# Optimization experiments

Hardware: AMD Instinct MI355X
Metric: run time of the kernel (lower is better)

Reference implementation:

```python
import jax, jax.numpy as jnp
import numpy as np

B, TE, TD, H = 4, 1024, 512, 128


def setup_inputs() -> dict:
    key = jax.random.key(0)
    k1, k2, k3, k4, k5 = jax.random.split(key, 5)
    return {
        "encoder_out": jax.random.normal(k1, (B, TE, H), dtype=jnp.float32),
        "decoder_out": jax.random.normal(k2, (B, TD, H), dtype=jnp.float32),
        "W_a": jax.random.normal(k3, (H, H), dtype=jnp.float32) * 0.05,
        "U_a": jax.random.normal(k4, (H, H), dtype=jnp.float32) * 0.05,
        "V_a": jax.random.normal(k5, (H, 1), dtype=jnp.float32) * 0.05,
    }


def reference(encoder_out, decoder_out, W_a, U_a, V_a):
    # Bahdanau additive attention, vectorized over all decoder steps at once.
    # (The original K.rnn loop has no true recurrence; steps are independent.)
    W_s = jnp.einsum('bth,hk->btk', encoder_out, W_a)   # [B, Te, H]
    U_h = jnp.einsum('bdh,hk->bdk', decoder_out, U_a)   # [B, Td, H]
    # energies: v^T tanh(W s_t + U h_d) -> [B, Td, Te]
    tanh_arg = jnp.tanh(W_s[:, None, :, :] + U_h[:, :, None, :])  # [B, Td, Te, H]
    e = jnp.einsum('bdth,ho->bdt', tanh_arg, V_a)
    e = jax.nn.softmax(e, axis=-1)                      # attention weights [B, Td, Te]
    # context vectors: weighted sum over encoder positions -> [B, Td, H]
    c = jnp.einsum('bdt,bth->bdh', e, encoder_out)
    return (c, e)
```

## Files before the change

kernel.cpp:

```cpp
#include <hip/hip_runtime.h>

#define BB    4
#define TE    1024
#define TD    512
#define HH    128
#define DTILE 4
#define TTILE 64
#define ESTR  (TE + 8)
#define LOG2E 1.4426950408889634f

typedef float f32x2 __attribute__((ext_vector_type(2)));

__device__ __forceinline__ f32x2 pk_fma(f32x2 a, f32x2 b, f32x2 c) {
    return __builtin_elementwise_fma(a, b, c);
}

__device__ __forceinline__ float tanh_eval(float x) {
    float e = __builtin_amdgcn_exp2f(2.0f * LOG2E * x);
    return 1.0f - 2.0f * __builtin_amdgcn_rcpf(e + 1.0f);
}

__global__ __launch_bounds__(512) void proj_gemm(
    const float* __restrict__ enc, const float* __restrict__ dec,
    const float* __restrict__ Wa,  const float* __restrict__ Ua,
    float* __restrict__ out)
{
    __shared__ float Xs[16 * HH];

    const int tid = threadIdx.x;
    const int r0  = blockIdx.x * 16;

    const float* X; const float* W; int rX0;
    if (r0 < BB * TE) { X = enc; W = Wa; rX0 = r0; }
    else              { X = dec; W = Ua; rX0 = r0 - BB * TE; }

    {
        const int r = tid >> 5, c = tid & 31;
        *(float4*)&Xs[r * HH + c * 4] =
            *(const float4*)&X[(size_t)(rX0 + r) * HH + c * 4];
    }
    __syncthreads();

    const int rr = tid >> 5;
    const int c4 = tid & 31;

    f32x2 aL0 = {0.f, 0.f}, aH0 = {0.f, 0.f};
    f32x2 aL1 = {0.f, 0.f}, aH1 = {0.f, 0.f};

    const float* Wc   = W + c4 * 4;
    const float* xrow = &Xs[rr * HH];

    #pragma unroll 4
    for (int k = 0; k < HH; k += 4) {
        float4 w0 = *(const float4*)&Wc[(k + 0) * HH];
        float4 w1 = *(const float4*)&Wc[(k + 1) * HH];
        float4 w2 = *(const float4*)&Wc[(k + 2) * HH];
        float4 w3 = *(const float4*)&Wc[(k + 3) * HH];
        float4 xv = *(const float4*)&xrow[k];

        aL0 = pk_fma((f32x2){xv.x, xv.x}, (f32x2){w0.x, w0.y}, aL0);
        aH0 = pk_fma((f32x2){xv.x, xv.x}, (f32x2){w0.z, w0.w}, aH0);
        aL1 = pk_fma((f32x2){xv.y, xv.y}, (f32x2){w1.x, w1.y}, aL1);
        aH1 = pk_fma((f32x2){xv.y, xv.y}, (f32x2){w1.z, w1.w}, aH1);
        aL0 = pk_fma((f32x2){xv.z, xv.z}, (f32x2){w2.x, w2.y}, aL0);
        aH0 = pk_fma((f32x2){xv.z, xv.z}, (f32x2){w2.z, w2.w}, aH0);
        aL1 = pk_fma((f32x2){xv.w, xv.w}, (f32x2){w3.x, w3.y}, aL1);
        aH1 = pk_fma((f32x2){xv.w, xv.w}, (f32x2){w3.z, w3.w}, aH1);
    }

    f32x2 aL = aL0 + aL1;
    f32x2 aH = aH0 + aH1;

    float4 o;
    o.x = tanh_eval(aL.x); o.y = tanh_eval(aL.y);
    o.z = tanh_eval(aH.x); o.w = tanh_eval(aH.y);
    *(float4*)&out[(size_t)(r0 + rr) * HH + c4 * 4] = o;
}

__global__ __launch_bounds__(512, 4) void attn_fused(
    const float* __restrict__ enc,
    const float* __restrict__ ta,
    const float* __restrict__ tb,
    const float* __restrict__ Va,
    float* __restrict__ c_out,
    float* __restrict__ e_out)
{
    __shared__ float e_s[DTILE * ESTR];
    __shared__ float c_red[8 * DTILE * HH];

    const int tid = threadIdx.x;
    const int l   = tid & 63;
    const int w   = tid >> 6;
    const int b   = blockIdx.x >> 7;
    const int d0  = (blockIdx.x & 127) * DTILE;

    {
        const int g  = l >> 3;
        const int hl = l & 7;
        const int dl = g & 3;
        const int rh = g >> 2;

        f32x2 Bl[4], Bh[4], Pl[4], Ph[4], Vl[4], Vh[4];
        #pragma unroll
        for (int j = 0; j < 4; ++j) {
            float4 vv = *(const float4*)&Va[(j * 8 + hl) * 4];
            float4 bb = *(const float4*)&tb[((size_t)b * TD + d0 + dl) * HH + (j * 8 + hl) * 4];
            Vl[j] = (f32x2){vv.x, vv.y};  Vh[j] = (f32x2){vv.z, vv.w};
            Bl[j] = (f32x2){bb.x, bb.y};  Bh[j] = (f32x2){bb.z, bb.w};
            Pl[j] = Vl[j] * Bl[j];        Ph[j] = Vh[j] * Bh[j];
        }

        const float* ta_b = ta + (size_t)b * TE * HH;

        auto rowOf = [&](int i) {
            return ((i >> 2) << 6) + w * 8 + ((i & 3) << 1) + rh;
        };

        float4 A0[4], A1[4];
        auto loadA = [&](int i, float4 (&A)[4]) {
            const float* base = ta_b + (size_t)rowOf(i) * HH;
            #pragma unroll
            for (int j = 0; j < 4; ++j)
                A[j] = *(const float4*)&base[(j * 8 + hl) * 4];
        };

        auto p1c = [&](int i, float4 (&A)[4]) {
            const f32x2 one2 = {1.0f, 1.0f};
            f32x2 n2[8], d2[8];
            #pragma unroll
            for (int j = 0; j < 4; ++j) {
                f32x2 Al = (f32x2){A[j].x, A[j].y};
                f32x2 Ah = (f32x2){A[j].z, A[j].w};
                n2[2 * j]     = pk_fma(Vl[j], Al, Pl[j]);
                n2[2 * j + 1] = pk_fma(Vh[j], Ah, Ph[j]);
                d2[2 * j]     = pk_fma(Al, Bl[j], one2);
                d2[2 * j + 1] = pk_fma(Ah, Bh[j], one2);
            }
            #pragma unroll
            for (int s = 4; s >= 1; s >>= 1) {
                #pragma unroll
                for (int k = 0; k < s; ++k) {
                    n2[k] = pk_fma(n2[2 * k], d2[2 * k + 1], n2[2 * k + 1] * d2[2 * k]);
                    d2[k] = d2[2 * k] * d2[2 * k + 1];
                }
            }
            float num = n2[0].x * d2[0].y + n2[0].y * d2[0].x;
            float den = d2[0].x * d2[0].y;
            float e = num * __builtin_amdgcn_rcpf(den);
            e += __shfl_xor(e, 1);
            e += __shfl_xor(e, 2);
            e += __shfl_xor(e, 4);
            if (hl == 0) e_s[dl * ESTR + rowOf(i)] = e;
        };

        loadA(0, A0);
        #pragma unroll 1
        for (int i = 0; i < 62; i += 2) {
            loadA(i + 1, A1);
            p1c(i, A0);
            loadA(i + 2, A0);
            p1c(i + 1, A1);
        }
        loadA(63, A1);
        p1c(62, A0);
        p1c(63, A1);
    }
    __syncthreads();

    {
        const int d2 = w & 3, hf = w >> 2;
        float ev[16];
        float m = -3.0e38f;
        #pragma unroll
        for (int i = 0; i < 16; ++i) {
            ev[i] = e_s[d2 * ESTR + i * 64 + l];
            m = fmaxf(m, ev[i]);
        }
        #pragma unroll
        for (int off = 32; off; off >>= 1) m = fmaxf(m, __shfl_xor(m, off));
        float s = 0.f;
        #pragma unroll
        for (int i = 0; i < 16; ++i) {
            ev[i] = __builtin_amdgcn_exp2f((ev[i] - m) * LOG2E);
            s += ev[i];
        }
        #pragma unroll
        for (int off = 32; off; off >>= 1) s += __shfl_xor(s, off);
        float inv = __builtin_amdgcn_rcpf(s);

        __syncthreads();
        float* eo = e_out + ((size_t)b * TD + d0 + d2) * TE;
        #pragma unroll
        for (int i = 0; i < 8; ++i) {
            int ii = hf * 8 + i;
            float p = ev[ii] * inv;
            e_s[d2 * ESTR + ii * 64 + l] = p;
            eo[ii * 64 + l] = p;
        }
        __syncthreads();
    }

    const int h4 = l & 31, tsub = l >> 5;
    f32x2 accL[DTILE], accH[DTILE];
    #pragma unroll
    for (int d = 0; d < DTILE; ++d) {
        accL[d] = (f32x2){0.f, 0.f};
        accH[d] = (f32x2){0.f, 0.f};
    }

    {
        const float* enc_w = enc + ((size_t)b * TE + w * 8) * HH;
        float4 X0[4], X1[4];

        auto loadX = [&](int tt, float4 (&X)[4]) {
            const float* base = enc_w + (size_t)tt * TTILE * HH;
            #pragma unroll
            for (int k = 0; k < 4; ++k)
                X[k] = *(const float4*)&base[(tsub * 4 + k) * HH + h4 * 4];
        };

        auto p3c = [&](int tt, float4 (&X)[4]) {
            float4 ep[DTILE];
            #pragma unroll
            for (int d = 0; d < DTILE; ++d)
                ep[d] = *(const float4*)&e_s[d * ESTR + tt * TTILE + w * 8 + tsub * 4];
            #pragma unroll
            for (int k = 0; k < 4; ++k) {
                f32x2 xL = (f32x2){X[k].x, X[k].y};
                f32x2 xH = (f32x2){X[k].z, X[k].w};
                #pragma unroll
                for (int d = 0; d < DTILE; ++d) {
                    float p = k == 0 ? ep[d].x : k == 1 ? ep[d].y
                            : k == 2 ? ep[d].z : ep[d].w;
                    f32x2 pv = (f32x2){p, p};
                    accL[d] = pk_fma(pv, xL, accL[d]);
                    accH[d] = pk_fma(pv, xH, accH[d]);
                }
            }
        };

        loadX(0, X0);
        #pragma unroll 1
        for (int tt = 0; tt < 14; tt += 2) {
            loadX(tt + 1, X1);
            p3c(tt, X0);
            loadX(tt + 2, X0);
            p3c(tt + 1, X1);
        }
        loadX(15, X1);
        p3c(14, X0);
        p3c(15, X1);
    }

    float4 acc4[DTILE];
    #pragma unroll
    for (int d = 0; d < DTILE; ++d)
        acc4[d] = make_float4(accL[d].x, accL[d].y, accH[d].x, accH[d].y);
    #pragma unroll
    for (int d = 0; d < DTILE; ++d) {
        acc4[d].x += __shfl_xor(acc4[d].x, 32);
        acc4[d].y += __shfl_xor(acc4[d].y, 32);
        acc4[d].z += __shfl_xor(acc4[d].z, 32);
        acc4[d].w += __shfl_xor(acc4[d].w, 32);
    }
    if (tsub == 0) {
        #pragma unroll
        for (int d = 0; d < DTILE; ++d)
            *(float4*)&c_red[(w * DTILE + d) * HH + h4 * 4] = acc4[d];
    }
    __syncthreads();

    if (w < DTILE && l < 32) {
        float4 o = make_float4(0.f, 0.f, 0.f, 0.f);
        #pragma unroll
        for (int ww = 0; ww < 8; ++ww) {
            float4 p = *(const float4*)&c_red[(ww * DTILE + w) * HH + l * 4];
            o.x += p.x; o.y += p.y; o.z += p.z; o.w += p.w;
        }
        *(float4*)&c_out[((size_t)b * TD + d0 + w) * HH + l * 4] = o;
    }
}

extern "C" void kernel_launch(void* const* d_in, const int* in_sizes, int n_in,
                              void* d_out, int out_size, void* d_ws, size_t ws_size,
                              hipStream_t stream) {
    (void)in_sizes; (void)n_in; (void)out_size; (void)ws_size;

    const float* enc = (const float*)d_in[0];
    const float* dec = (const float*)d_in[1];
    const float* Wa  = (const float*)d_in[2];
    const float* Ua  = (const float*)d_in[3];
    const float* Va  = (const float*)d_in[4];

    float* c_out = (float*)d_out;
    float* e_out = (float*)d_out + BB * TD * HH;

    float* proj = (float*)d_ws;
    float* ta_p = proj;
    float* tb_p = proj + BB * TE * HH;

    proj_gemm<<<384, 512, 0, stream>>>(enc, dec, Wa, Ua, proj);
    attn_fused<<<(BB * TD) / DTILE, 512, 0, stream>>>(enc, ta_p, tb_p, Va, c_out, e_out);
}
```

Measured before the change: 131.0 us.

## Double attention block threads and stagger projection K loop start

```diff
diff --git a/kernel.cpp b/kernel.cpp
--- a/kernel.cpp
+++ b/kernel.cpp
@@ -25,33 +25,24 @@
     const float* __restrict__ Wa,  const float* __restrict__ Ua,
     float* __restrict__ out)
 {
-    __shared__ float Xs[16 * HH];
-
     const int tid = threadIdx.x;
-    const int r0  = blockIdx.x * 16;
+    const int bid = blockIdx.x;
+    const int r0  = bid * 16;
 
     const float* X; const float* W; int rX0;
     if (r0 < BB * TE) { X = enc; W = Wa; rX0 = r0; }
     else              { X = dec; W = Ua; rX0 = r0 - BB * TE; }
 
-    {
-        const int r = tid >> 5, c = tid & 31;
-        *(float4*)&Xs[r * HH + c * 4] =
-            *(const float4*)&X[(size_t)(rX0 + r) * HH + c * 4];
-    }
-    __syncthreads();
-
     const int rr = tid >> 5;
     const int c4 = tid & 31;
 
+    const float* xrow = X + (size_t)(rX0 + rr) * HH;
+    const float* Wc   = W + c4 * 4;
+
     f32x2 aL0 = {0.f, 0.f}, aH0 = {0.f, 0.f};
     f32x2 aL1 = {0.f, 0.f}, aH1 = {0.f, 0.f};
 
-    const float* Wc   = W + c4 * 4;
-    const float* xrow = &Xs[rr * HH];
-
-    #pragma unroll 4
-    for (int k = 0; k < HH; k += 4) {
+    auto body = [&](int k) {
         float4 w0 = *(const float4*)&Wc[(k + 0) * HH];
         float4 w1 = *(const float4*)&Wc[(k + 1) * HH];
         float4 w2 = *(const float4*)&Wc[(k + 2) * HH];
@@ -66,7 +57,13 @@
         aH0 = pk_fma((f32x2){xv.z, xv.z}, (f32x2){w2.z, w2.w}, aH0);
         aL1 = pk_fma((f32x2){xv.w, xv.w}, (f32x2){w3.x, w3.y}, aL1);
         aH1 = pk_fma((f32x2){xv.w, xv.w}, (f32x2){w3.z, w3.w}, aH1);
-    }
+    };
+
+    const int k0 = (bid & 31) * 4;
+    #pragma unroll 4
+    for (int k = k0; k < HH; k += 4) body(k);
+    #pragma unroll 4
+    for (int k = 0; k < k0; k += 4) body(k);
 
     f32x2 aL = aL0 + aL1;
     f32x2 aH = aH0 + aH1;
@@ -77,7 +74,7 @@
     *(float4*)&out[(size_t)(r0 + rr) * HH + c4 * 4] = o;
 }
 
-__global__ __launch_bounds__(512, 4) void attn_fused(
+__global__ __launch_bounds__(1024, 8) void attn_fused(
     const float* __restrict__ enc,
     const float* __restrict__ ta,
     const float* __restrict__ tb,
@@ -86,7 +83,7 @@
     float* __restrict__ e_out)
 {
     __shared__ float e_s[DTILE * ESTR];
-    __shared__ float c_red[8 * DTILE * HH];
+    __shared__ float c_red[16 * DTILE * HH];
 
     const int tid = threadIdx.x;
     const int l   = tid & 63;
@@ -95,6 +92,8 @@
     const int d0  = (blockIdx.x & 127) * DTILE;
 
     {
+        const int w2 = w & 7;
+        const int ih = w >> 3;
         const int g  = l >> 3;
         const int hl = l & 7;
         const int dl = g & 3;
@@ -113,7 +112,7 @@
         const float* ta_b = ta + (size_t)b * TE * HH;
 
         auto rowOf = [&](int i) {
-            return ((i >> 2) << 6) + w * 8 + ((i & 3) << 1) + rh;
+            return ((i >> 2) << 6) + w2 * 8 + ((i & 3) << 1) + rh;
         };
 
         float4 A0[4], A1[4];
@@ -153,22 +152,23 @@
             if (hl == 0) e_s[dl * ESTR + rowOf(i)] = e;
         };
 
-        loadA(0, A0);
+        const int i0 = ih * 32;
+        loadA(i0, A0);
         #pragma unroll 1
-        for (int i = 0; i < 62; i += 2) {
+        for (int i = i0; i < i0 + 30; i += 2) {
             loadA(i + 1, A1);
             p1c(i, A0);
             loadA(i + 2, A0);
             p1c(i + 1, A1);
         }
-        loadA(63, A1);
-        p1c(62, A0);
-        p1c(63, A1);
+        loadA(i0 + 31, A1);
+        p1c(i0 + 30, A0);
+        p1c(i0 + 31, A1);
     }
     __syncthreads();
 
     {
-        const int d2 = w & 3, hf = w >> 2;
+        const int d2 = w & 3, q = w >> 2;
         float ev[16];
         float m = -3.0e38f;
         #pragma unroll
@@ -191,8 +191,8 @@
         __syncthreads();
         float* eo = e_out + ((size_t)b * TD + d0 + d2) * TE;
         #pragma unroll
-        for (int i = 0; i < 8; ++i) {
-            int ii = hf * 8 + i;
+        for (int i = 0; i < 4; ++i) {
+            int ii = q * 4 + i;
             float p = ev[ii] * inv;
             e_s[d2 * ESTR + ii * 64 + l] = p;
             eo[ii * 64 + l] = p;
@@ -209,29 +209,28 @@
     }
 
     {
-        const float* enc_w = enc + ((size_t)b * TE + w * 8) * HH;
-        float4 X0[4], X1[4];
-
-        auto loadX = [&](int tt, float4 (&X)[4]) {
+        const float* enc_w = enc + ((size_t)b * TE + w * 4) * HH;
+        float4 X0[2], X1[2];
+
+        auto loadX = [&](int tt, float4 (&Xr)[2]) {
             const float* base = enc_w + (size_t)tt * TTILE * HH;
             #pragma unroll
-            for (int k = 0; k < 4; ++k)
-                X[k] = *(const float4*)&base[(tsub * 4 + k) * HH + h4 * 4];
-        };
-
-        auto p3c = [&](int tt, float4 (&X)[4]) {
-            float4 ep[DTILE];
+            for (int k = 0; k < 2; ++k)
+                Xr[k] = *(const float4*)&base[(tsub * 2 + k) * HH + h4 * 4];
+        };
+
+        auto p3c = [&](int tt, float4 (&Xr)[2]) {
+            f32x2 ep[DTILE];
             #pragma unroll
             for (int d = 0; d < DTILE; ++d)
-                ep[d] = *(const float4*)&e_s[d * ESTR + tt * TTILE + w * 8 + tsub * 4];
-            #pragma unroll
-            for (int k = 0; k < 4; ++k) {
-                f32x2 xL = (f32x2){X[k].x, X[k].y};
-                f32x2 xH = (f32x2){X[k].z, X[k].w};
+                ep[d] = *(const f32x2*)&e_s[d * ESTR + tt * TTILE + w * 4 + tsub * 2];
+            #pragma unroll
+            for (int k = 0; k < 2; ++k) {
+                f32x2 xL = (f32x2){Xr[k].x, Xr[k].y};
+                f32x2 xH = (f32x2){Xr[k].z, Xr[k].w};
                 #pragma unroll
                 for (int d = 0; d < DTILE; ++d) {
-                    float p = k == 0 ? ep[d].x : k == 1 ? ep[d].y
-                            : k == 2 ? ep[d].z : ep[d].w;
+                    float p = (k == 0) ? ep[d].x : ep[d].y;
                     f32x2 pv = (f32x2){p, p};
                     accL[d] = pk_fma(pv, xL, accL[d]);
                     accH[d] = pk_fma(pv, xH, accH[d]);
@@ -273,7 +272,7 @@
     if (w < DTILE && l < 32) {
         float4 o = make_float4(0.f, 0.f, 0.f, 0.f);
         #pragma unroll
-        for (int ww = 0; ww < 8; ++ww) {
+        for (int ww = 0; ww < 16; ++ww) {
             float4 p = *(const float4*)&c_red[(ww * DTILE + w) * HH + l * 4];
             o.x += p.x; o.y += p.y; o.z += p.z; o.w += p.w;
         }
@@ -300,5 +299,5 @@
     float* tb_p = proj + BB * TE * HH;
 
     proj_gemm<<<384, 512, 0, stream>>>(enc, dec, Wa, Ua, proj);
-    attn_fused<<<(BB * TD) / DTILE, 512, 0, stream>>>(enc, ta_p, tb_p, Va, c_out, e_out);
-}
+    attn_fused<<<(BB * TD) / DTILE, 1024, 0, stream>>>(enc, ta_p, tb_p, Va, c_out, e_out);
+}
```

Measured after the change: 344.3 us. 163% more time.
